# Performance work log

Measured on AMD Instinct MI355X. Metric: run time of the kernel, lower is better.

The kernel has to match this reference:

```python
import jax, jax.numpy as jnp
import numpy as np

MAX_DISPARITY = 192


def _cost_volume(L, R, D):
    """Banded stereo correlation.

    cost[n, j, h, x] = sum_c L[n,c,h,x] * R[n,c,h,x-j], zero when x < j.
    Equivalent to the original full (W,W) matmul followed by per-disparity
    diagonal extraction + left zero-pad, but computed as D shifted
    dot-products (honors the banded structure).
    """
    N, C, H, W = L.shape
    Rp = jnp.pad(R, ((0, 0), (0, 0), (0, 0), (D - 1, 0)))  # left zero-pad

    def step(_, j):
        Rs = jax.lax.dynamic_slice_in_dim(Rp, D - 1 - j, W, axis=3)  # R shifted right by j
        c = jnp.einsum('nchw,nchw->nhw', L, Rs)
        return None, c

    _, cv = jax.lax.scan(step, None, jnp.arange(D))  # (D, N, H, W)
    return jnp.transpose(cv, (1, 0, 2, 3))  # (N, D, H, W)


def setup_inputs() -> dict:
    key = jax.random.key(0)
    ks = jax.random.split(key, 6)
    shapes = [(1, 32, 256, 512), (1, 32, 128, 256), (1, 32, 64, 128)]
    inp = {}
    for i, s in enumerate(shapes):
        inp[f'left{i}'] = jax.random.normal(ks[2 * i], s, dtype=jnp.float32)
        inp[f'right{i}'] = jax.random.normal(ks[2 * i + 1], s, dtype=jnp.float32)
    return inp


def reference(left0, right0, left1, right1, left2, right2):
    lefts = [left0, left1, left2]
    rights = [right0, right1, right2]
    max_disparity = min(MAX_DISPARITY, lefts[0].shape[-1])
    cost_volumes = []
    for i, (L, R) in enumerate(zip(lefts, rights)):
        D = max_disparity // (2 ** i)
        cost_volumes.append(_cost_volume(L, R, D))
    return tuple(cost_volumes)
```

## Files before the change

kernel.cpp:

```cpp
#include <hip/hip_runtime.h>


#define TX 128
#define TJ 128
#define NCS 16
#define NSTG 2

typedef float vf4 __attribute__((ext_vector_type(4)));

__device__ __forceinline__ int swz64(int q) { return q ^ ((q >> 3) & 7); }
__device__ __forceinline__ int swz32(int q) { return q ^ ((q >> 3) & 3); }

#define NBLK_TOTAL 2368

__global__ __launch_bounds__(256, 4)
void cost_volume_fused(const float* __restrict__ L0, const float* __restrict__ R0,
                       const float* __restrict__ L1, const float* __restrict__ R1,
                       const float* __restrict__ L2, const float* __restrict__ R2,
                       float* __restrict__ out)
{
    __shared__ float Ls[NCS * TX];
    __shared__ float Rs[NCS * (TX + TJ)];

    const int id = blockIdx.x;
    const float* L; const float* R; float* o;
    int H, W, D, bx, by, h;
    if (id < 2048) {
        L = L0; R = R0; o = out;
        H = 256; W = 512; D = 192;
        bx = id & 3; by = (id >> 2) & 1; h = id >> 3;
    } else if (id < 2304) {
        int r = id - 2048;
        L = L1; R = R1; o = out + (size_t)192 * 256 * 512;
        H = 128; W = 256; D = 96;
        bx = r & 1; by = 0; h = r >> 1;
    } else {
        int r = id - 2304;
        L = L2; R = R2; o = out + (size_t)192 * 256 * 512 + (size_t)96 * 128 * 256;
        H = 64; W = 128; D = 48;
        bx = 0; by = 0; h = r;
    }

    const int x0 = bx * TX;
    const int j0 = by * TJ;
    const int t  = threadIdx.x;
    const int tx = t & 15;
    const int ty = t >> 4;
    const int jbase = j0 + ty * 8;

    if (x0 + TX - 1 < j0) {
        const vf4 z = (vf4)(0.f);
        #pragma unroll
        for (int jj = 0; jj < 8; ++jj) {
            int j = jbase + jj;
            if (j < D) {
                float* p = o + ((size_t)j * H + h) * W + x0;
                __builtin_nontemporal_store(z, (vf4*)(p + 4 * tx));
                __builtin_nontemporal_store(z, (vf4*)(p + 64 + 4 * tx));
            }
        }
        return;
    }

    const bool active = (jbase < D);
    const size_t HW = (size_t)H * W;
    const float* Lb = L + (size_t)h * W;
    const float* Rb = R + (size_t)h * W;
    const int gbase = x0 - j0 - TJ;

    float acc[8][8];
    #pragma unroll
    for (int jj = 0; jj < 8; ++jj)
        #pragma unroll
        for (int xx = 0; xx < 8; ++xx) acc[jj][xx] = 0.f;

    const int loA = 4 * swz32(tx);
    const int loB = 4 * swz32(tx + 16);
    const int tA  = tx - 2 * ty;
    const int roA0 = 4 * swz64(tA + 30);
    const int roA1 = 4 * swz64(tA + 31);
    const int roA2 = 4 * swz64(tA + 32);
    const int roB0 = 4 * swz64(tA + 46);
    const int roB1 = 4 * swz64(tA + 47);
    const int roB2 = 4 * swz64(tA + 48);

    #pragma unroll
    for (int s = 0; s < NSTG; ++s) {
        const int c0 = s * NCS;
        #pragma unroll
        for (int k = 0; k < 2; ++k) {
            int f = t + k * 256;
            int c = f >> 5, q = f & 31;
            vf4 v = *(const vf4*)(Lb + (size_t)(c0 + c) * HW + x0 + 4 * q);
            *(vf4*)&Ls[c * TX + 4 * swz32(q)] = v;
        }
        #pragma unroll
        for (int k = 0; k < 4; ++k) {
            int f = t + k * 256;
            int c = f >> 6, q = f & 63;
            int g = gbase + 4 * q;
            vf4 v = (vf4)(0.f);
            if (g >= 0 && g < W)
                v = *(const vf4*)(Rb + (size_t)(c0 + c) * HW + g);
            *(vf4*)&Rs[c * (TX + TJ) + 4 * swz64(q)] = v;
        }
        __syncthreads();

        if (active) {
            #pragma unroll 1
            for (int c = 0; c < NCS; ++c) {
                const float* Lc = Ls + c * TX;
                const float* Rc = Rs + c * (TX + TJ);
                float lA[4], lB[4], rA[12], rB[12];
                *(vf4*)&lA[0] = *(const vf4*)(Lc + loA);
                *(vf4*)&lB[0] = *(const vf4*)(Lc + loB);
                *(vf4*)&rA[0] = *(const vf4*)(Rc + roA0);
                *(vf4*)&rA[4] = *(const vf4*)(Rc + roA1);
                *(vf4*)&rA[8] = *(const vf4*)(Rc + roA2);
                *(vf4*)&rB[0] = *(const vf4*)(Rc + roB0);
                *(vf4*)&rB[4] = *(const vf4*)(Rc + roB1);
                *(vf4*)&rB[8] = *(const vf4*)(Rc + roB2);
                #pragma unroll
                for (int jj = 0; jj < 8; ++jj)
                    #pragma unroll
                    for (int i = 0; i < 4; ++i) {
                        acc[jj][i]     = fmaf(lA[i], rA[8 + i - jj], acc[jj][i]);
                        acc[jj][4 + i] = fmaf(lB[i], rB[8 + i - jj], acc[jj][4 + i]);
                    }
            }
        }
        if (s + 1 < NSTG) __syncthreads();
    }

    if (active) {
        #pragma unroll
        for (int jj = 0; jj < 8; ++jj) {
            int j = jbase + jj;
            if (j < D) {
                float* p = o + ((size_t)j * H + h) * W + x0;
                vf4 va = {acc[jj][0], acc[jj][1], acc[jj][2], acc[jj][3]};
                vf4 vb = {acc[jj][4], acc[jj][5], acc[jj][6], acc[jj][7]};
                __builtin_nontemporal_store(va, (vf4*)(p + 4 * tx));
                __builtin_nontemporal_store(vb, (vf4*)(p + 64 + 4 * tx));
            }
        }
    }
}

extern "C" void kernel_launch(void* const* d_in, const int* in_sizes, int n_in,
                              void* d_out, int out_size, void* d_ws, size_t ws_size,
                              hipStream_t stream)
{
    const float* L0 = (const float*)d_in[0];
    const float* R0 = (const float*)d_in[1];
    const float* L1 = (const float*)d_in[2];
    const float* R1 = (const float*)d_in[3];
    const float* L2 = (const float*)d_in[4];
    const float* R2 = (const float*)d_in[5];
    float* out = (float*)d_out;

    cost_volume_fused<<<dim3(NBLK_TOTAL), dim3(256), 0, stream>>>(
        L0, R0, L1, R1, L2, R2, out);
}
```

Before: 183.5 us.

## Cover full disparity range per block with 24-disparity-per-thread register tiles

Each block now covers all disparities for a 128-wide x tile instead of splitting disparities across two blocks, which halves the block count and removes redundant L loads. Each thread computes 24 disparities by 4 x positions from one 28-float sliding window of R, raising FMA-to-LDS-load ratio. Threads whose tile lies entirely in the zero region skip the compute but still store zeros. Swizzled LDS indexing is dropped and occupancy hints go down to 2 blocks per CU, which may add bank conflicts and lower latency hiding.

Result: faster. 179.8 us (-2.0%).

```diff
diff --git a/kernel.cpp b/kernel.cpp
--- a/kernel.cpp
+++ b/kernel.cpp
@@ -2,87 +2,65 @@
 
 
 #define TX 128
-#define TJ 128
+#define TJ 192
+#define JT 24
 #define NCS 16
 #define NSTG 2
+#define LSW 128
+#define RSW 320
+
+#define NBLK_TOTAL 1344
 
 typedef float vf4 __attribute__((ext_vector_type(4)));
 
-__device__ __forceinline__ int swz64(int q) { return q ^ ((q >> 3) & 7); }
-__device__ __forceinline__ int swz32(int q) { return q ^ ((q >> 3) & 3); }
-
-#define NBLK_TOTAL 2368
-
-__global__ __launch_bounds__(256, 4)
+__global__ __launch_bounds__(256, 2)
 void cost_volume_fused(const float* __restrict__ L0, const float* __restrict__ R0,
                        const float* __restrict__ L1, const float* __restrict__ R1,
                        const float* __restrict__ L2, const float* __restrict__ R2,
                        float* __restrict__ out)
 {
-    __shared__ float Ls[NCS * TX];
-    __shared__ float Rs[NCS * (TX + TJ)];
+    __shared__ float Ls[NCS * LSW];
+    __shared__ float Rs[NCS * RSW];
 
     const int id = blockIdx.x;
     const float* L; const float* R; float* o;
-    int H, W, D, bx, by, h;
-    if (id < 2048) {
+    int H, W, D, bx, h;
+    if (id < 1024) {
         L = L0; R = R0; o = out;
         H = 256; W = 512; D = 192;
-        bx = id & 3; by = (id >> 2) & 1; h = id >> 3;
-    } else if (id < 2304) {
-        int r = id - 2048;
+        bx = id & 3; h = id >> 2;
+    } else if (id < 1280) {
+        int r = id - 1024;
         L = L1; R = R1; o = out + (size_t)192 * 256 * 512;
         H = 128; W = 256; D = 96;
-        bx = r & 1; by = 0; h = r >> 1;
+        bx = r & 1; h = r >> 1;
     } else {
-        int r = id - 2304;
+        int r = id - 1280;
         L = L2; R = R2; o = out + (size_t)192 * 256 * 512 + (size_t)96 * 128 * 256;
         H = 64; W = 128; D = 48;
-        bx = 0; by = 0; h = r;
+        bx = 0; h = r;
     }
 
     const int x0 = bx * TX;
-    const int j0 = by * TJ;
     const int t  = threadIdx.x;
-    const int tx = t & 15;
-    const int ty = t >> 4;
-    const int jbase = j0 + ty * 8;
+    const int tx = t & 31;
+    const int ty = t >> 5;
+    const int jbase = ty * JT;
 
-    if (x0 + TX - 1 < j0) {
-        const vf4 z = (vf4)(0.f);
-        #pragma unroll
-        for (int jj = 0; jj < 8; ++jj) {
-            int j = jbase + jj;
-            if (j < D) {
-                float* p = o + ((size_t)j * H + h) * W + x0;
-                __builtin_nontemporal_store(z, (vf4*)(p + 4 * tx));
-                __builtin_nontemporal_store(z, (vf4*)(p + 64 + 4 * tx));
-            }
-        }
-        return;
-    }
-
-    const bool active = (jbase < D);
     const size_t HW = (size_t)H * W;
     const float* Lb = L + (size_t)h * W;
     const float* Rb = R + (size_t)h * W;
-    const int gbase = x0 - j0 - TJ;
 
-    float acc[8][8];
+    const bool active = (jbase < D);
+    const bool live   = active && (x0 + 4 * tx + 3 >= jbase);
+
+    float acc[JT][4];
     #pragma unroll
-    for (int jj = 0; jj < 8; ++jj)
-        #pragma unroll
-        for (int xx = 0; xx < 8; ++xx) acc[jj][xx] = 0.f;
+    for (int jj = 0; jj < JT; ++jj) {
+        acc[jj][0] = 0.f; acc[jj][1] = 0.f; acc[jj][2] = 0.f; acc[jj][3] = 0.f;
+    }
 
-    const int loA = 4 * swz32(tx);
-    const int loB = 4 * swz32(tx + 16);
-    const int tA  = tx - 2 * ty;
-    const int roA0 = 4 * swz64(tA + 30);
-    const int roA1 = 4 * swz64(tA + 31);
-    const int roA2 = 4 * swz64(tA + 32);
-    const int roB0 = 4 * swz64(tA + 46);
-    const int roB1 = 4 * swz64(tA + 47);
-    const int roB2 = 4 * swz64(tA + 48);
+    const int rbase = 4 * tx - JT * ty + (TJ - 24);
 
     #pragma unroll
     for (int s = 0; s < NSTG; ++s) {
@@ -92,41 +70,36 @@
             int f = t + k * 256;
             int c = f >> 5, q = f & 31;
             vf4 v = *(const vf4*)(Lb + (size_t)(c0 + c) * HW + x0 + 4 * q);
-            *(vf4*)&Ls[c * TX + 4 * swz32(q)] = v;
+            *(vf4*)&Ls[c * LSW + 4 * q] = v;
         }
         #pragma unroll
-        for (int k = 0; k < 4; ++k) {
+        for (int k = 0; k < 5; ++k) {
             int f = t + k * 256;
-            int c = f >> 6, q = f & 63;
-            int g = gbase + 4 * q;
+            int c = f / 80;
+            int q = f - 80 * c;
+            int g = x0 - TJ + 4 * q;
             vf4 v = (vf4)(0.f);
             if (g >= 0 && g < W)
                 v = *(const vf4*)(Rb + (size_t)(c0 + c) * HW + g);
-            *(vf4*)&Rs[c * (TX + TJ) + 4 * swz64(q)] = v;
+            *(vf4*)&Rs[c * RSW + 4 * q] = v;
         }
         __syncthreads();
 
-        if (active) {
+        if (live) {
             #pragma unroll 1
             for (int c = 0; c < NCS; ++c) {
-                const float* Lc = Ls + c * TX;
-                const float* Rc = Rs + c * (TX + TJ);
-                float lA[4], lB[4], rA[12], rB[12];
-                *(vf4*)&lA[0] = *(const vf4*)(Lc + loA);
-                *(vf4*)&lB[0] = *(const vf4*)(Lc + loB);
-                *(vf4*)&rA[0] = *(const vf4*)(Rc + roA0);
-                *(vf4*)&rA[4] = *(const vf4*)(Rc + roA1);
-                *(vf4*)&rA[8] = *(const vf4*)(Rc + roA2);
-                *(vf4*)&rB[0] = *(const vf4*)(Rc + roB0);
-                *(vf4*)&rB[4] = *(const vf4*)(Rc + roB1);
-                *(vf4*)&rB[8] = *(const vf4*)(Rc + roB2);
+                const float* Lc = Ls + c * LSW;
+                const float* Rc = Rs + c * RSW + rbase;
+                float lv[4], rw[28];
+                *(vf4*)&lv[0] = *(const vf4*)(Lc + 4 * tx);
                 #pragma unroll
-                for (int jj = 0; jj < 8; ++jj)
+                for (int k = 0; k < 7; ++k)
+                    *(vf4*)&rw[4 * k] = *(const vf4*)(Rc + 4 * k);
+                #pragma unroll
+                for (int jj = 0; jj < JT; ++jj)
                     #pragma unroll
-                    for (int i = 0; i < 4; ++i) {
-                        acc[jj][i]     = fmaf(lA[i], rA[8 + i - jj], acc[jj][i]);
-                        acc[jj][4 + i] = fmaf(lB[i], rB[8 + i - jj], acc[jj][4 + i]);
-                    }
+                    for (int i = 0; i < 4; ++i)
+                        acc[jj][i] = fmaf(lv[i], rw[24 + i - jj], acc[jj][i]);
             }
         }
         if (s + 1 < NSTG) __syncthreads();
@@ -134,15 +107,11 @@
 
     if (active) {
         #pragma unroll
-        for (int jj = 0; jj < 8; ++jj) {
+        for (int jj = 0; jj < JT; ++jj) {
             int j = jbase + jj;
-            if (j < D) {
-                float* p = o + ((size_t)j * H + h) * W + x0;
-                vf4 va = {acc[jj][0], acc[jj][1], acc[jj][2], acc[jj][3]};
-                vf4 vb = {acc[jj][4], acc[jj][5], acc[jj][6], acc[jj][7]};
-                __builtin_nontemporal_store(va, (vf4*)(p + 4 * tx));
-                __builtin_nontemporal_store(vb, (vf4*)(p + 64 + 4 * tx));
-            }
+            float* p = o + ((size_t)j * H + h) * W + x0 + 4 * tx;
+            vf4 v = {acc[jj][0], acc[jj][1], acc[jj][2], acc[jj][3]};
+            __builtin_nontemporal_store(v, (vf4*)p);
         }
     }
 }
```
